# Optimization experiments

Hardware: AMD Instinct MI355X
Metric: run time of the kernel (lower is better)

Reference implementation:

```python
import jax, jax.numpy as jnp
import numpy as np
from jax import lax

H, W = 4096, 4096

def setup_inputs() -> dict:
    key = jax.random.key(0)
    k_occ, k_seed = jax.random.split(key)
    occupied = (jax.random.uniform(k_occ, (H, W)) < 0.3).astype(jnp.float32)
    flood = ((jax.random.uniform(k_seed, (H, W)) < 1e-3).astype(jnp.float32)
             * (1.0 - occupied))
    flood_input = jnp.stack([occupied, flood], axis=-1)  # [H, W, 2]
    flood_count = jnp.zeros((H, W), dtype=jnp.float32)
    # Fixed flood kernel, HWIO layout: (3, 3, in=2, out=1)
    kernel = jnp.zeros((3, 3, 2, 1), dtype=jnp.float32)
    kernel = kernel.at[1, 1, 0, 0].set(-5.0)  # occupied center blocks flood
    kernel = kernel.at[1, 2, 1, 0].set(1.0)   # right
    kernel = kernel.at[2, 1, 1, 0].set(1.0)   # down
    kernel = kernel.at[1, 0, 1, 0].set(1.0)   # left
    kernel = kernel.at[0, 1, 1, 0].set(1.0)   # up
    kernel = kernel.at[1, 1, 1, 0].set(1.0)   # center
    bias = jnp.zeros((1,), dtype=jnp.float32)
    return {"flood_input": flood_input, "flood_count": flood_count,
            "kernel": kernel, "bias": bias, "num_steps": 16}

def reference(flood_input, flood_count, kernel, bias, num_steps):
    dn = ("NHWC", "HWIO", "NHWC")

    def flood_step(carry, _):
        x, count = carry                      # x: [H, W, 2], count: [H, W]
        occupied = x[..., 0]
        y = lax.conv_general_dilated(x[None], kernel, (1, 1), "SAME",
                                     dimension_numbers=dn)[0, ..., 0] + bias[0]
        y = jnp.clip(y, 0.0, 1.0)             # flooded frontier
        new_x = jnp.stack([occupied, y], axis=-1)
        return (new_x, count + y), None

    (x_final, count_final), _ = lax.scan(flood_step,
                                         (flood_input, flood_count),
                                         None, length=num_steps)
    # [H, W, 3]: occupied, flood, count
    return jnp.concatenate([x_final, count_final[..., None]], axis=-1)
```

## Files before the change

kernel.cpp:

```cpp
#include <hip/hip_runtime.h>


typedef unsigned long long u64;

#define HH 4096
#define WW 4096
#define WPR 64
#define NSTEPS 16
#define VROWS 224
#define RROWS 256

__global__ __launch_bounds__(256) void pack_kernel(
    const float* __restrict__ in, u64* __restrict__ occP, u64* __restrict__ flP)
{
    const int lane = threadIdx.x & 63;
    const int wv   = threadIdx.x >> 6;
    const int r    = blockIdx.x;
#pragma unroll
    for (int b = 0; b < 2; ++b) {
        float vx[8], vy[8];
#pragma unroll
        for (int j = 0; j < 8; ++j) {
            const int w = wv * 16 + b * 8 + j;
            const float2 v = *(const float2*)(in + ((size_t)r * WW + (w << 6) + lane) * 2);
            vx[j] = v.x; vy[j] = v.y;
        }
#pragma unroll
        for (int j = 0; j < 8; ++j) {
            const int w = wv * 16 + b * 8 + j;
            const u64 om = __ballot(vx[j] > 0.5f);
            const u64 fm = __ballot(vy[j] > 0.5f);
            if (lane == 0) {
                occP[(size_t)w * HH + r] = om;
                flP [(size_t)w * HH + r] = fm;
            }
        }
    }
}

__global__ __launch_bounds__(256) void flood_kernel(
    const u64* __restrict__ occP, const u64* __restrict__ flP,
    u64* __restrict__ planes)
{
    __shared__ u64 bufA[RROWS * 2];
    __shared__ u64 bufB[RROWS * 2];

    const int tid = threadIdx.x;
    const int w   = blockIdx.x;
    const int gr  = blockIdx.y * VROWS + tid - 16;
    const bool rin = (gr >= 0) && (gr < HH);

    u64 oc[3], fl[3];
#pragma unroll
    for (int j = 0; j < 3; ++j) {
        const int q = w - 1 + j;
        const bool v = rin && (q >= 0) && (q < WPR);
        oc[j] = v ? occP[(size_t)q * HH + gr] : ~0ull;
        fl[j] = v ? flP [(size_t)q * HH + gr] : 0ull;
    }
    const u64 nocc0 = ~((oc[0] >> 48) | (oc[1] << 16));
    const u64 nocc1 = ~((oc[1] >> 48) | (oc[2] << 16));
    u64 f0 = (fl[0] >> 48) | (fl[1] << 16);
    u64 f1 = (fl[1] >> 48) | (fl[2] << 16);

    u64 c00 = 0, c01 = 0, c02 = 0, c03 = 0, c04 = 0;
    u64 c10 = 0, c11 = 0, c12 = 0, c13 = 0, c14 = 0;

    bufA[tid * 2 + 0] = f0; bufA[tid * 2 + 1] = f1;
    __syncthreads();

    u64* cur = bufA;
    u64* nxt = bufB;
    for (int it = 0; it < NSTEPS; ++it) {
        u64 up0 = 0, up1 = 0, dn0 = 0, dn1 = 0;
        if (tid > 0)         { up0 = cur[(tid - 1) * 2 + 0]; up1 = cur[(tid - 1) * 2 + 1]; }
        if (tid < RROWS - 1) { dn0 = cur[(tid + 1) * 2 + 0]; dn1 = cur[(tid + 1) * 2 + 1]; }
        const u64 nf0 = nocc0 & (f0 | (f0 << 1) | (f0 >> 1) | (f1 << 63) | up0 | dn0);
        const u64 nf1 = nocc1 & (f1 | (f1 << 1) | (f0 >> 63) | (f1 >> 1) | up1 | dn1);
        u64 c, t;
        c = nf0;
        t = c00; c00 = t ^ c; c = t & c;
        t = c01; c01 = t ^ c; c = t & c;
        t = c02; c02 = t ^ c; c = t & c;
        t = c03; c03 = t ^ c; c = t & c;
        c04 ^= c;
        c = nf1;
        t = c10; c10 = t ^ c; c = t & c;
        t = c11; c11 = t ^ c; c = t & c;
        t = c12; c12 = t ^ c; c = t & c;
        t = c13; c13 = t ^ c; c = t & c;
        c14 ^= c;
        nxt[tid * 2 + 0] = nf0; nxt[tid * 2 + 1] = nf1;
        f0 = nf0; f1 = nf1;
        __syncthreads();
        u64* tmp = cur; cur = nxt; nxt = tmp;
    }

    if (tid >= 16 && tid < 16 + VROWS && gr < HH) {
        const size_t o = (size_t)w * HH + gr;
        const size_t P = (size_t)WPR * HH;
        planes[o]         = (f0  >> 16) | (f1  << 48);
        planes[P + o]     = (c00 >> 16) | (c10 << 48);
        planes[2 * P + o] = (c01 >> 16) | (c11 << 48);
        planes[3 * P + o] = (c02 >> 16) | (c12 << 48);
        planes[4 * P + o] = (c03 >> 16) | (c13 << 48);
        planes[5 * P + o] = (c04 >> 16) | (c14 << 48);
    }
}

__global__ __launch_bounds__(256) void expand_kernel(
    const u64* __restrict__ occP, const u64* __restrict__ planes,
    const float* __restrict__ fcount, float* __restrict__ out)
{
    const int lane = threadIdx.x & 63;
    const int wv   = threadIdx.x >> 6;
    const int w    = blockIdx.x;
    const int r0   = blockIdx.y * 64 + wv * 16;
    const size_t P = (size_t)WPR * HH;
    const size_t col = (size_t)(w << 6) + lane;

#pragma unroll 2
    for (int i = 0; i < 16; ++i) {
        const int r = r0 + i;
        const size_t o = (size_t)w * HH + r;
        const u64 ow = occP[o];
        const u64 fw = planes[o];
        const u64 q0 = planes[P + o];
        const u64 q1 = planes[2 * P + o];
        const u64 q2 = planes[3 * P + o];
        const u64 q3 = planes[4 * P + o];
        const u64 q4 = planes[5 * P + o];
        const float fc = fcount[(size_t)r * WW + col];
        const int cv = (int)((q0 >> lane) & 1ull)
                     + ((int)((q1 >> lane) & 1ull) << 1)
                     + ((int)((q2 >> lane) & 1ull) << 2)
                     + ((int)((q3 >> lane) & 1ull) << 3)
                     + ((int)((q4 >> lane) & 1ull) << 4);
        float3 o3;
        o3.x = (float)((ow >> lane) & 1ull);
        o3.y = (float)((fw >> lane) & 1ull);
        o3.z = (float)cv + fc;
        *(float3*)(out + ((size_t)r * WW + col) * 3) = o3;
    }
}

extern "C" void kernel_launch(void* const* d_in, const int* in_sizes, int n_in,
                              void* d_out, int out_size, void* d_ws, size_t ws_size,
                              hipStream_t stream) {
    const float* flood_input = (const float*)d_in[0];
    const float* flood_cnt   = (const float*)d_in[1];
    float* out = (float*)d_out;

    u64* occP   = (u64*)d_ws;
    u64* flP    = occP + (size_t)WPR * HH;
    u64* planes = flP  + (size_t)WPR * HH;

    pack_kernel<<<dim3(HH), dim3(256), 0, stream>>>(flood_input, occP, flP);
    flood_kernel<<<dim3(WPR, (HH + VROWS - 1) / VROWS), dim3(256), 0, stream>>>(
        occP, flP, planes);
    expand_kernel<<<dim3(WPR, HH / 64), dim3(256), 0, stream>>>(
        occP, planes, flood_cnt, out);
}
```

Before: 389.5 us.

## Fuse pack, flood and expand into one cooperative persistent kernel

Replaces three separate kernel launches with one cooperative kernel of 512 persistent blocks that loop over rows and tiles, using grid-wide syncs between the pack, flood and expand phases. This removes per-launch overhead and the kernel boundaries. In exchange, occupancy is capped by the fixed grid. The expand phase now walks rows per block instead of 2D tiles, which changes its memory access pattern: the u64 plane reads become strided.

New measurement: 651.3 us. +67.2%, slower.

```diff
diff --git a/kernel.cpp b/kernel.cpp
--- a/kernel.cpp
+++ b/kernel.cpp
@@ -1,146 +1,150 @@
 #include <hip/hip_runtime.h>
+#include <hip/hip_cooperative_groups.h>
 
 
 typedef unsigned long long u64;
+namespace cg = cooperative_groups;
 
 #define HH 4096
 #define WW 4096
 #define WPR 64
 #define NSTEPS 16
+#define NBLK 512
+#define NTILES 1216
 #define VROWS 224
 #define RROWS 256
 
-__global__ __launch_bounds__(256) void pack_kernel(
-    const float* __restrict__ in, u64* __restrict__ occP, u64* __restrict__ flP)
+__global__ __launch_bounds__(256, 4) void fused_kernel(
+    const float* __restrict__ in, const float* __restrict__ fcount,
+    float* __restrict__ out,
+    u64* __restrict__ occP, u64* __restrict__ flP, u64* __restrict__ planes)
 {
-    const int lane = threadIdx.x & 63;
-    const int wv   = threadIdx.x >> 6;
-    const int r    = blockIdx.x;
+    __shared__ u64 bufA[RROWS * 2];
+    __shared__ u64 bufB[RROWS * 2];
+    cg::grid_group grid = cg::this_grid();
+
+    const int tid  = threadIdx.x;
+    const int lane = tid & 63;
+    const int wv   = tid >> 6;
+    const int bid  = blockIdx.x;
+    const size_t P = (size_t)WPR * HH;
+
+    for (int r = bid; r < HH; r += NBLK) {
 #pragma unroll
-    for (int b = 0; b < 2; ++b) {
-        float vx[8], vy[8];
+        for (int b = 0; b < 2; ++b) {
+            float vx[8], vy[8];
 #pragma unroll
-        for (int j = 0; j < 8; ++j) {
-            const int w = wv * 16 + b * 8 + j;
-            const float2 v = *(const float2*)(in + ((size_t)r * WW + (w << 6) + lane) * 2);
-            vx[j] = v.x; vy[j] = v.y;
-        }
+            for (int j = 0; j < 8; ++j) {
+                const int w = wv * 16 + b * 8 + j;
+                const float2 v = *(const float2*)(in + ((size_t)r * WW + (w << 6) + lane) * 2);
+                vx[j] = v.x; vy[j] = v.y;
+            }
 #pragma unroll
-        for (int j = 0; j < 8; ++j) {
-            const int w = wv * 16 + b * 8 + j;
-            const u64 om = __ballot(vx[j] > 0.5f);
-            const u64 fm = __ballot(vy[j] > 0.5f);
-            if (lane == 0) {
-                occP[(size_t)w * HH + r] = om;
-                flP [(size_t)w * HH + r] = fm;
+            for (int j = 0; j < 8; ++j) {
+                const int w = wv * 16 + b * 8 + j;
+                const u64 om = __ballot(vx[j] > 0.5f);
+                const u64 fm = __ballot(vy[j] > 0.5f);
+                if (lane == 0) {
+                    occP[(size_t)w * HH + r] = om;
+                    flP [(size_t)w * HH + r] = fm;
+                }
             }
         }
     }
-}
+    __threadfence();
+    grid.sync();
 
-__global__ __launch_bounds__(256) void flood_kernel(
-    const u64* __restrict__ occP, const u64* __restrict__ flP,
-    u64* __restrict__ planes)
-{
-    __shared__ u64 bufA[RROWS * 2];
-    __shared__ u64 bufB[RROWS * 2];
+    for (int t = bid; t < NTILES; t += NBLK) {
+        const int w  = t & 63;
+        const int ty = t >> 6;
+        const int gr = ty * VROWS + tid - 16;
+        const bool rin = (gr >= 0) && (gr < HH);
 
-    const int tid = threadIdx.x;
-    const int w   = blockIdx.x;
-    const int gr  = blockIdx.y * VROWS + tid - 16;
-    const bool rin = (gr >= 0) && (gr < HH);
+        u64 oc[3], fl[3];
+#pragma unroll
+        for (int j = 0; j < 3; ++j) {
+            const int q = w - 1 + j;
+            const bool v = rin && (q >= 0) && (q < WPR);
+            oc[j] = v ? occP[(size_t)q * HH + gr] : ~0ull;
+            fl[j] = v ? flP [(size_t)q * HH + gr] : 0ull;
+        }
+        const u64 nocc0 = ~((oc[0] >> 48) | (oc[1] << 16));
+        const u64 nocc1 = ~((oc[1] >> 48) | (oc[2] << 16));
+        u64 f0 = (fl[0] >> 48) | (fl[1] << 16);
+        u64 f1 = (fl[1] >> 48) | (fl[2] << 16);
 
-    u64 oc[3], fl[3];
-#pragma unroll
-    for (int j = 0; j < 3; ++j) {
-        const int q = w - 1 + j;
-        const bool v = rin && (q >= 0) && (q < WPR);
-        oc[j] = v ? occP[(size_t)q * HH + gr] : ~0ull;
-        fl[j] = v ? flP [(size_t)q * HH + gr] : 0ull;
+        u64 c00 = 0, c01 = 0, c02 = 0, c03 = 0, c04 = 0;
+        u64 c10 = 0, c11 = 0, c12 = 0, c13 = 0, c14 = 0;
+
+        __syncthreads();
+        bufA[tid * 2 + 0] = f0; bufA[tid * 2 + 1] = f1;
+        __syncthreads();
+
+        u64* cur = bufA;
+        u64* nxt = bufB;
+        for (int it = 0; it < NSTEPS; ++it) {
+            u64 up0 = 0, up1 = 0, dn0 = 0, dn1 = 0;
+            if (tid > 0)         { up0 = cur[(tid - 1) * 2 + 0]; up1 = cur[(tid - 1) * 2 + 1]; }
+            if (tid < RROWS - 1) { dn0 = cur[(tid + 1) * 2 + 0]; dn1 = cur[(tid + 1) * 2 + 1]; }
+            const u64 nf0 = nocc0 & (f0 | (f0 << 1) | (f0 >> 1) | (f1 << 63) | up0 | dn0);
+            const u64 nf1 = nocc1 & (f1 | (f1 << 1) | (f0 >> 63) | (f1 >> 1) | up1 | dn1);
+            u64 c, tt;
+            c = nf0;
+            tt = c00; c00 = tt ^ c; c = tt & c;
+            tt = c01; c01 = tt ^ c; c = tt & c;
+            tt = c02; c02 = tt ^ c; c = tt & c;
+            tt = c03; c03 = tt ^ c; c = tt & c;
+            c04 ^= c;
+            c = nf1;
+            tt = c10; c10 = tt ^ c; c = tt & c;
+            tt = c11; c11 = tt ^ c; c = tt & c;
+            tt = c12; c12 = tt ^ c; c = tt & c;
+            tt = c13; c13 = tt ^ c; c = tt & c;
+            c14 ^= c;
+            nxt[tid * 2 + 0] = nf0; nxt[tid * 2 + 1] = nf1;
+            f0 = nf0; f1 = nf1;
+            __syncthreads();
+            u64* tmp = cur; cur = nxt; nxt = tmp;
+        }
+
+        if (tid >= 16 && tid < 16 + VROWS && gr < HH) {
+            const size_t o = (size_t)w * HH + gr;
+            planes[o]         = (f0  >> 16) | (f1  << 48);
+            planes[P + o]     = (c00 >> 16) | (c10 << 48);
+            planes[2 * P + o] = (c01 >> 16) | (c11 << 48);
+            planes[3 * P + o] = (c02 >> 16) | (c12 << 48);
+            planes[4 * P + o] = (c03 >> 16) | (c13 << 48);
+            planes[5 * P + o] = (c04 >> 16) | (c14 << 48);
+        }
     }
-    const u64 nocc0 = ~((oc[0] >> 48) | (oc[1] << 16));
-    const u64 nocc1 = ~((oc[1] >> 48) | (oc[2] << 16));
-    u64 f0 = (fl[0] >> 48) | (fl[1] << 16);
-    u64 f1 = (fl[1] >> 48) | (fl[2] << 16);
+    __threadfence();
+    grid.sync();
 
-    u64 c00 = 0, c01 = 0, c02 = 0, c03 = 0, c04 = 0;
-    u64 c10 = 0, c11 = 0, c12 = 0, c13 = 0, c14 = 0;
-
-    bufA[tid * 2 + 0] = f0; bufA[tid * 2 + 1] = f1;
-    __syncthreads();
-
-    u64* cur = bufA;
-    u64* nxt = bufB;
-    for (int it = 0; it < NSTEPS; ++it) {
-        u64 up0 = 0, up1 = 0, dn0 = 0, dn1 = 0;
-        if (tid > 0)         { up0 = cur[(tid - 1) * 2 + 0]; up1 = cur[(tid - 1) * 2 + 1]; }
-        if (tid < RROWS - 1) { dn0 = cur[(tid + 1) * 2 + 0]; dn1 = cur[(tid + 1) * 2 + 1]; }
-        const u64 nf0 = nocc0 & (f0 | (f0 << 1) | (f0 >> 1) | (f1 << 63) | up0 | dn0);
-        const u64 nf1 = nocc1 & (f1 | (f1 << 1) | (f0 >> 63) | (f1 >> 1) | up1 | dn1);
-        u64 c, t;
-        c = nf0;
-        t = c00; c00 = t ^ c; c = t & c;
-        t = c01; c01 = t ^ c; c = t & c;
-        t = c02; c02 = t ^ c; c = t & c;
-        t = c03; c03 = t ^ c; c = t & c;
-        c04 ^= c;
-        c = nf1;
-        t = c10; c10 = t ^ c; c = t & c;
-        t = c11; c11 = t ^ c; c = t & c;
-        t = c12; c12 = t ^ c; c = t & c;
-        t = c13; c13 = t ^ c; c = t & c;
-        c14 ^= c;
-        nxt[tid * 2 + 0] = nf0; nxt[tid * 2 + 1] = nf1;
-        f0 = nf0; f1 = nf1;
-        __syncthreads();
-        u64* tmp = cur; cur = nxt; nxt = tmp;
-    }
-
-    if (tid >= 16 && tid < 16 + VROWS && gr < HH) {
-        const size_t o = (size_t)w * HH + gr;
-        const size_t P = (size_t)WPR * HH;
-        planes[o]         = (f0  >> 16) | (f1  << 48);
-        planes[P + o]     = (c00 >> 16) | (c10 << 48);
-        planes[2 * P + o] = (c01 >> 16) | (c11 << 48);
-        planes[3 * P + o] = (c02 >> 16) | (c12 << 48);
-        planes[4 * P + o] = (c03 >> 16) | (c13 << 48);
-        planes[5 * P + o] = (c04 >> 16) | (c14 << 48);
-    }
-}
-
-__global__ __launch_bounds__(256) void expand_kernel(
-    const u64* __restrict__ occP, const u64* __restrict__ planes,
-    const float* __restrict__ fcount, float* __restrict__ out)
-{
-    const int lane = threadIdx.x & 63;
-    const int wv   = threadIdx.x >> 6;
-    const int w    = blockIdx.x;
-    const int r0   = blockIdx.y * 64 + wv * 16;
-    const size_t P = (size_t)WPR * HH;
-    const size_t col = (size_t)(w << 6) + lane;
-
+    for (int r = bid; r < HH; r += NBLK) {
 #pragma unroll 2
-    for (int i = 0; i < 16; ++i) {
-        const int r = r0 + i;
-        const size_t o = (size_t)w * HH + r;
-        const u64 ow = occP[o];
-        const u64 fw = planes[o];
-        const u64 q0 = planes[P + o];
-        const u64 q1 = planes[2 * P + o];
-        const u64 q2 = planes[3 * P + o];
-        const u64 q3 = planes[4 * P + o];
-        const u64 q4 = planes[5 * P + o];
-        const float fc = fcount[(size_t)r * WW + col];
-        const int cv = (int)((q0 >> lane) & 1ull)
-                     + ((int)((q1 >> lane) & 1ull) << 1)
-                     + ((int)((q2 >> lane) & 1ull) << 2)
-                     + ((int)((q3 >> lane) & 1ull) << 3)
-                     + ((int)((q4 >> lane) & 1ull) << 4);
-        float3 o3;
-        o3.x = (float)((ow >> lane) & 1ull);
-        o3.y = (float)((fw >> lane) & 1ull);
-        o3.z = (float)cv + fc;
-        *(float3*)(out + ((size_t)r * WW + col) * 3) = o3;
+        for (int i = 0; i < 16; ++i) {
+            const int w2 = wv * 16 + i;
+            const size_t o = (size_t)w2 * HH + r;
+            const u64 ow = occP[o];
+            const u64 fw = planes[o];
+            const u64 q0 = planes[P + o];
+            const u64 q1 = planes[2 * P + o];
+            const u64 q2 = planes[3 * P + o];
+            const u64 q3 = planes[4 * P + o];
+            const u64 q4 = planes[5 * P + o];
+            const size_t col = (size_t)(w2 << 6) + lane;
+            const float fc = fcount[(size_t)r * WW + col];
+            const int cv = (int)((q0 >> lane) & 1ull)
+                         + ((int)((q1 >> lane) & 1ull) << 1)
+                         + ((int)((q2 >> lane) & 1ull) << 2)
+                         + ((int)((q3 >> lane) & 1ull) << 3)
+                         + ((int)((q4 >> lane) & 1ull) << 4);
+            float3 o3;
+            o3.x = (float)((ow >> lane) & 1ull);
+            o3.y = (float)((fw >> lane) & 1ull);
+            o3.z = (float)cv + fc;
+            *(float3*)(out + ((size_t)r * WW + col) * 3) = o3;
+        }
     }
 }
 
@@ -155,9 +159,8 @@
     u64* flP    = occP + (size_t)WPR * HH;
     u64* planes = flP  + (size_t)WPR * HH;
 
-    pack_kernel<<<dim3(HH), dim3(256), 0, stream>>>(flood_input, occP, flP);
-    flood_kernel<<<dim3(WPR, (HH + VROWS - 1) / VROWS), dim3(256), 0, stream>>>(
-        occP, flP, planes);
-    expand_kernel<<<dim3(WPR, HH / 64), dim3(256), 0, stream>>>(
-        occP, planes, flood_cnt, out);
+    void* args[] = { (void*)&flood_input, (void*)&flood_cnt, (void*)&out,
+                     (void*)&occP, (void*)&flP, (void*)&planes };
+    hipLaunchCooperativeKernel((const void*)fused_kernel, dim3(NBLK), dim3(256),
+                               args, 0, stream);
 }
```
